# Optimization experiments

Hardware: AMD Instinct MI355X
Metric: run time of the kernel (lower is better)

## Reference

```python
import jax, jax.numpy as jnp
import numpy as np
from jax import lax

THRESHOLD = 0.9


def _conv(x, w, b, stride):
    # x: [B,C,H,W], w: [O,I,3,3] (OIHW)
    y = lax.conv_general_dilated(x, w, (stride, stride), 'SAME',
                                 dimension_numbers=('NCHW', 'OIHW', 'NCHW'))
    return y + b[None, :, None, None]


def _expert(x, w1, b1, w2, b2, wf, bf):
    h = jax.nn.relu(_conv(x, w1, b1, 2))   # [B,64,112,112]
    h = jax.nn.relu(_conv(h, w2, b2, 2))   # [B,128,56,56]
    g = h.mean(axis=(2, 3))                # [B,128] global average pool
    return g @ wf + bf                     # [B,2] logits


def setup_inputs() -> dict:
    key = jax.random.key(0)
    ks = jax.random.split(key, 13)
    f32 = jnp.float32
    def rn(k, shape, scale):
        return jax.random.normal(k, shape, dtype=f32) * scale
    return {
        'x':    rn(ks[0], (64, 3, 224, 224), 1.0),
        't_w1': rn(ks[1], (64, 3, 3, 3),   0.2),
        't_b1': jnp.zeros((64,), f32),
        't_w2': rn(ks[2], (128, 64, 3, 3), 0.05),
        't_b2': jnp.zeros((128,), f32),
        't_wf': rn(ks[3], (128, 2),        0.1),
        't_bf': jnp.zeros((2,), f32),
        'f_w1': rn(ks[4], (64, 3, 3, 3),   0.2),
        'f_b1': jnp.zeros((64,), f32),
        'f_w2': rn(ks[5], (128, 64, 3, 3), 0.05),
        'f_b2': jnp.zeros((128,), f32),
        'f_wf': rn(ks[6], (128, 2),        0.1),
        'f_bf': jnp.zeros((2,), f32),
    }


def reference(x, t_w1, t_b1, t_w2, t_b2, t_wf, t_bf,
              f_w1, f_b1, f_w2, f_b2, f_wf, f_bf):
    t_logits = _expert(x, t_w1, t_b1, t_w2, t_b2, t_wf, t_bf)   # [B,2]
    t_conf = jax.nn.softmax(t_logits, axis=1).max(axis=1)        # [B]
    use_texture2 = t_conf <= THRESHOLD                           # [B] bool
    # jit-friendly dense evaluation of the second expert; the where-mask
    # reproduces the original gather/scatter blend exactly (values and grads).
    f_logits = _expert(x, f_w1, f_b1, f_w2, f_b2, f_wf, f_bf)   # [B,2]
    output = jnp.where(use_texture2[:, None],
                       0.7 * t_logits + 0.3 * f_logits,
                       t_logits)
    freq_usage = use_texture2.astype(jnp.float32).mean()
    return (output, freq_usage)
```

## Files before the change

kernel.cpp:

```cpp
#include <hip/hip_runtime.h>
#include <hip/hip_bf16.h>
#include <math.h>


#define W2B_OFF   0ull
#define W1F_OFF   589824ull
#define G_OFF     606208ull
#define H1_OFF    671744ull
#define H1E_US    52301824ull
#define H1B_US    817216ull
#define WS_NEED   (H1_OFF + 2ull*H1E_US*2ull + 4096ull)

typedef __attribute__((ext_vector_type(8))) short bf16x8;
typedef __attribute__((ext_vector_type(4))) float f32x4;

__device__ inline ushort f2bf(float v) {
  __hip_bfloat16 h = __float2bfloat16(v);
  return *(ushort*)&h;
}
__device__ inline float bf2f(ushort u) {
  __hip_bfloat16 h = *(__hip_bfloat16*)&u;
  return __bfloat162float(h);
}

__global__ __launch_bounds__(256) void prep_new(
    const float* __restrict__ w2_t, const float* __restrict__ w2_f,
    const float* __restrict__ w1_t, const float* __restrict__ w1_f,
    char* __restrict__ ws) {
  int idx = blockIdx.x * 256 + threadIdx.x;
  ushort* w2frag = (ushort*)(ws + W2B_OFF);
  ushort* w1frag = (ushort*)(ws + W1F_OFF);
  if (idx < 294912) {
    int j    = idx & 7;
    int lane = (idx >> 3) & 63;
    int t2   = idx >> 9;
    int kc   = t2 % 18;
    int t3   = t2 / 18;
    int octile = t3 & 7;
    int t4   = t3 >> 3;
    int e    = t4 & 1;
    int term = t4 >> 1;
    int oc = octile * 16 + (lane & 15);
    int kk = kc * 32 + (lane >> 4) * 8 + j;
    int kh = kk / 192, r2 = kk - kh * 192, kw = r2 >> 6, ic = r2 & 63;
    const float* src = e ? w2_f : w2_t;
    float w = src[((oc * 64 + ic) * 3 + kh) * 3 + kw];
    ushort hi = f2bf(w);
    w2frag[idx] = term ? f2bf(w - bf2f(hi)) : hi;
  } else if (idx < 294912 + 8192) {
    int i2   = idx - 294912;
    int j    = i2 & 7;
    int lane = (i2 >> 3) & 63;
    int m    = (i2 >> 9) & 3;
    int term = (i2 >> 11) & 1;
    int e    = (i2 >> 12) & 1;
    int oc = m * 16 + (lane & 15);
    int kk = (lane >> 4) * 8 + j;
    const float* src = e ? w1_f : w1_t;
    float w = (kk < 27) ? src[oc * 27 + kk] : 0.f;
    ushort hi = f2bf(w);
    w1frag[i2] = term ? f2bf(w - bf2f(hi)) : hi;
  }
}

__global__ __launch_bounds__(256) void conv1_mfma(
    const float* __restrict__ x,
    const ushort* __restrict__ w1f_all,
    const float* __restrict__ b1_t, const float* __restrict__ b1_f,
    ushort* __restrict__ h1_all)
{
  const int gR  = blockIdx.x;
  const int b   = blockIdx.y;
  const int e   = blockIdx.z;
  const int tid = threadIdx.x;
  const int w    = tid >> 6;
  const int lane = tid & 63;
  const int q    = lane >> 4;
  const int n    = lane & 15;

  ushort* h1b = h1_all + (size_t)e * H1E_US + (size_t)b * H1B_US;
  const float* b1 = e ? b1_f : b1_t;

  constexpr int CW = 233;
  __shared__ unsigned int xs[3 * 9 * CW];

  const float* xb = x + (size_t)b * 150528;
  const int xr0 = 8 * gR;
  for (int i = tid; i < 1512; i += 256) {
    int ic  = i / 504;
    int rem = i - ic * 504;
    int r   = rem / 56;
    int u   = rem - r * 56;
    int xr  = xr0 + r;
    float4 p = make_float4(0.f, 0.f, 0.f, 0.f);
    if (xr < 224) p = *(const float4*)(xb + (ic * 224 + xr) * 224 + 4 * u);
    float vv[4] = {p.x, p.y, p.z, p.w};
    int base = (ic * 9 + r) * CW + 4 * u;
#pragma unroll
    for (int jj = 0; jj < 4; ++jj) {
      ushort hi = f2bf(vv[jj]);
      ushort lo = f2bf(vv[jj] - bf2f(hi));
      xs[base + jj] = (unsigned int)hi | ((unsigned int)lo << 16);
    }
  }
  if (tid < 27) xs[tid * CW + 224] = 0;

  h1b[((size_t)((4 * gR + (tid >> 6)) * 113 + 112)) * 64 + (tid & 63)] = 0;
  if (gR == 0) {
    unsigned int* z = (unsigned int*)&h1b[(size_t)112 * 113 * 64];
    for (int i = tid; i < 3616; i += 256) z[i] = 0;
  }

  bf16x8 whi[4], wlo[4];
#pragma unroll
  for (int m = 0; m < 4; ++m) {
    whi[m] = *(const bf16x8*)&w1f_all[(((size_t)(e * 2 + 0) * 4 + m) * 64 + lane) * 8];
    wlo[m] = *(const bf16x8*)&w1f_all[(((size_t)(e * 2 + 1) * 4 + m) * 64 + lane) * 8];
  }
  float4 bv[4];
#pragma unroll
  for (int m = 0; m < 4; ++m)
    bv[m] = *(const float4*)&b1[m * 16 + 4 * q];

  int off[8];
#pragma unroll
  for (int j = 0; j < 8; ++j) {
    int kk = q * 8 + j;
    if (kk < 27) {
      int ic = kk / 9;
      int r9 = kk - ic * 9;
      int kh = r9 / 3;
      int kw = r9 - kh * 3;
      off[j] = (ic * 9 + kh) * CW + kw;
    } else {
      off[j] = -1;
    }
  }

  __syncthreads();

  const int row   = 4 * gR + w;
  const int rbase = (2 * w) * CW;

  for (int nt = 0; nt < 7; ++nt) {
    const int c = nt * 16 + n;
    const int base = rbase + 2 * c;
    unsigned int g[8];
#pragma unroll
    for (int j = 0; j < 8; ++j)
      g[j] = (off[j] >= 0) ? xs[base + off[j]] : 0u;
    bf16x8 bhi, blo;
#pragma unroll
    for (int j = 0; j < 8; ++j) {
      bhi[j] = (short)(g[j] & 0xffffu);
      blo[j] = (short)(g[j] >> 16);
    }
    f32x4 acc[4];
#pragma unroll
    for (int m = 0; m < 4; ++m) acc[m] = (f32x4){0.f, 0.f, 0.f, 0.f};
#pragma unroll
    for (int m = 0; m < 4; ++m) {
      acc[m] = __builtin_amdgcn_mfma_f32_16x16x32_bf16(whi[m], bhi, acc[m], 0, 0, 0);
      acc[m] = __builtin_amdgcn_mfma_f32_16x16x32_bf16(wlo[m], bhi, acc[m], 0, 0, 0);
      acc[m] = __builtin_amdgcn_mfma_f32_16x16x32_bf16(whi[m], blo, acc[m], 0, 0, 0);
    }
    size_t po = ((size_t)(row * 113 + c)) * 64 + 4 * q;
#pragma unroll
    for (int m = 0; m < 4; ++m) {
      float v0 = fmaxf(acc[m][0] + bv[m].x, 0.f);
      float v1 = fmaxf(acc[m][1] + bv[m].y, 0.f);
      float v2 = fmaxf(acc[m][2] + bv[m].z, 0.f);
      float v3 = fmaxf(acc[m][3] + bv[m].w, 0.f);
      uint2 uu;
      uu.x = (unsigned int)f2bf(v0) | ((unsigned int)f2bf(v1) << 16);
      uu.y = (unsigned int)f2bf(v2) | ((unsigned int)f2bf(v3) << 16);
      *(uint2*)&h1b[po + m * 16] = uu;
    }
  }
}

__global__ __launch_bounds__(256) void conv2_mfma(
    const ushort* __restrict__ h1_all,
    const ushort* __restrict__ w2frag,
    const float* __restrict__ b2_t, const float* __restrict__ b2_f,
    float* __restrict__ g)
{
  const int T = blockIdx.x;
  const int b = blockIdx.y;
  const int e = blockIdx.z;
  const int tid  = threadIdx.x;
  const int w    = tid >> 6;
  const int lane = tid & 63;
  const ushort* h1b = h1_all + (size_t)e * H1E_US + (size_t)b * H1B_US;
  const float* b2 = e ? b2_f : b2_t;

  __shared__ ushort hs[2 * 113 * 72];

  const int q   = lane >> 4;
  const int n   = lane & 15;
  const int pxl = lane & 7;
  const int rl  = (lane >> 3) & 1;

  f32x4 acc[2][7];
#pragma unroll
  for (int mt = 0; mt < 2; ++mt)
#pragma unroll
    for (int nt = 0; nt < 7; ++nt) acc[mt][nt] = (f32x4){0.f, 0.f, 0.f, 0.f};

  for (int kh = 0; kh < 3; ++kh) {
    __syncthreads();
    for (int i = tid; i < 1808; i += 256) {
      int rs = (i >= 904) ? 1 : 0;
      int rem = i - rs * 904;
      int hx = rem >> 3, gq = rem & 7;
      int R = 4 * T + kh + 2 * rs;
      *(bf16x8*)&hs[(rs * 113 + hx) * 72 + 8 * gq] =
          *(const bf16x8*)&h1b[((size_t)(R * 113 + hx)) * 64 + 8 * gq];
    }
    __syncthreads();
#pragma unroll
    for (int kw = 0; kw < 3; ++kw) {
#pragma unroll
      for (int icc = 0; icc < 2; ++icc) {
        const int kc = kh * 6 + kw * 2 + icc;
        const int icoff = icc * 32 + 8 * q;
        bf16x8 bf[7];
#pragma unroll
        for (int nt = 0; nt < 7; ++nt) {
          int hx = 2 * (8 * nt + pxl) + kw;
          bf[nt] = *(const bf16x8*)&hs[(rl * 113 + hx) * 72 + icoff];
        }
#pragma unroll
        for (int term = 0; term < 2; ++term) {
#pragma unroll
          for (int mt = 0; mt < 2; ++mt) {
            const int octile = 2 * w + mt;
            bf16x8 af = *(const bf16x8*)
                &w2frag[((size_t)(((term * 2 + e) * 8 + octile) * 18 + kc)) * 512
                        + lane * 8];
#pragma unroll
            for (int nt = 0; nt < 7; ++nt)
              acc[mt][nt] = __builtin_amdgcn_mfma_f32_16x16x32_bf16(
                  af, bf[nt], acc[mt][nt], 0, 0, 0);
          }
        }
      }
    }
  }

#pragma unroll
  for (int mt = 0; mt < 2; ++mt) {
#pragma unroll
    for (int reg = 0; reg < 4; ++reg) {
      const int oc = 32 * w + 16 * mt + 4 * q + reg;
      const float bias = b2[oc];
      float s = 0.f;
#pragma unroll
      for (int nt = 0; nt < 7; ++nt) s += fmaxf(acc[mt][nt][reg] + bias, 0.f);
      s += __shfl_xor(s, 1);
      s += __shfl_xor(s, 2);
      s += __shfl_xor(s, 4);
      s += __shfl_xor(s, 8);
      if (n == 0) atomicAdd(&g[((size_t)e * 64 + b) * 128 + oc], s);
    }
  }
}

__global__ __launch_bounds__(64) void finale(
    const float* __restrict__ g,
    const float* __restrict__ t_wf, const float* __restrict__ t_bf,
    const float* __restrict__ f_wf, const float* __restrict__ f_bf,
    float* __restrict__ out)
{
  const int b = threadIdx.x;
  const float inv = 1.0f / 3136.0f;
  const float* gt = g + b * 128;
  const float* gf = g + (64 + b) * 128;
  float lt0 = t_bf[0], lt1 = t_bf[1];
  float lf0 = f_bf[0], lf1 = f_bf[1];
  for (int k = 0; k < 128; ++k) {
    float vt = gt[k] * inv;
    float vf = gf[k] * inv;
    lt0 = fmaf(vt, t_wf[2 * k],     lt0);
    lt1 = fmaf(vt, t_wf[2 * k + 1], lt1);
    lf0 = fmaf(vf, f_wf[2 * k],     lf0);
    lf1 = fmaf(vf, f_wf[2 * k + 1], lf1);
  }
  float m  = fmaxf(lt0, lt1);
  float e0 = expf(lt0 - m), e1 = expf(lt1 - m);
  float conf = fmaxf(e0, e1) / (e0 + e1);
  bool use2 = (conf <= 0.9f);
  out[2 * b]     = use2 ? 0.7f * lt0 + 0.3f * lf0 : lt0;
  out[2 * b + 1] = use2 ? 0.7f * lt1 + 0.3f * lf1 : lt1;
  unsigned long long mask = __ballot(use2);
  if (b == 0) out[128] = (float)__popcll(mask) * (1.0f / 64.0f);
}

__global__ __launch_bounds__(256) void transpose_w2(
    const float* __restrict__ w2_t, const float* __restrict__ w2_f,
    float* __restrict__ w2t) {
  int idx = blockIdx.x * 256 + threadIdx.x;
  int e = idx / 73728;
  int r = idx - e * 73728;
  int k = r >> 7, oc = r & 127;
  const float* src = e ? w2_f : w2_t;
  w2t[idx] = src[oc * 576 + k];
}

__global__ __launch_bounds__(256, 3) void fused_expert(
    const float* __restrict__ x,
    const float* __restrict__ w1_t, const float* __restrict__ b1_t,
    const float* __restrict__ b2_t,
    const float* __restrict__ w1_f, const float* __restrict__ b1_f,
    const float* __restrict__ b2_f,
    const float* __restrict__ w2t_all, float* __restrict__ g)
{
  const int tile = blockIdx.x, b = blockIdx.y, e = blockIdx.z;
  const int ty = tile >> 1, tx = tile & 1;
  const float* w1  = e ? w1_f : w1_t;
  const float* b1  = e ? b1_f : b1_t;
  const float* b2  = e ? b2_f : b2_t;
  const float* w2t = w2t_all + e * 73728;
  __shared__ float x_s[3 * 19 * 116];
  __shared__ float h1_s[8 * 9 * 58];
  __shared__ float w1_s[1728];
  const int tid = threadIdx.x;
  {
    const float* xb = x + (size_t)b * 150528;
    const int xr0 = ty * 16, xc0 = tx * 112;
    for (int idx = tid; idx < 3 * 19 * 116; idx += 256) {
      int ic = idx / (19 * 116);
      int rem = idx - ic * (19 * 116);
      int r = rem / 116, cc = rem - r * 116;
      int xr = xr0 + r, xc = xc0 + cc;
      float v = 0.f;
      if (xr < 224 && xc < 224 && cc < 115) v = xb[(ic * 224 + xr) * 224 + xc];
      x_s[idx] = v;
    }
    for (int idx = tid; idx < 1728; idx += 256) w1_s[idx] = w1[idx];
  }
  const int ocg = tid >> 4, posg = tid & 15;
  int pbase[7];
#pragma unroll
  for (int j = 0; j < 7; ++j) {
    int p = posg + 16 * j, py = p / 28, px = p - py * 28;
    pbase[j] = py * 2 * 58 + px * 2;
  }
  float acc[7][8];
#pragma unroll
  for (int j = 0; j < 7; ++j)
#pragma unroll
    for (int i = 0; i < 8; ++i) acc[j][i] = 0.f;
  const int hc_l = tid >> 5, l32 = tid & 31;
  for (int c = 0; c < 8; ++c) {
    __syncthreads();
    {
      const int hc = c * 8 + hc_l;
      const float bias = b1[hc];
      float wr[27];
#pragma unroll
      for (int qq = 0; qq < 27; ++qq) wr[qq] = w1_s[hc * 27 + qq];
      for (int p = l32; p < 513; p += 32) {
        int hy = p / 57, hx = p - hy * 57;
        float a = bias;
#pragma unroll
        for (int ic = 0; ic < 3; ++ic)
#pragma unroll
          for (int kh = 0; kh < 3; ++kh) {
            const float* row = &x_s[ic * (19 * 116) + (2 * hy + kh) * 116 + 2 * hx];
            a = fmaf(row[0], wr[ic * 9 + kh * 3 + 0], a);
            a = fmaf(row[1], wr[ic * 9 + kh * 3 + 1], a);
            a = fmaf(row[2], wr[ic * 9 + kh * 3 + 2], a);
          }
        float v = fmaxf(a, 0.f);
        int hy_g = ty * 8 + hy, hx_g = tx * 56 + hx;
        if (hy_g >= 112 || hx_g >= 112) v = 0.f;
        h1_s[hc_l * 522 + hy * 58 + hx] = v;
      }
    }
    __syncthreads();
    for (int ic_l = 0; ic_l < 8; ++ic_l) {
#pragma unroll
      for (int kh = 0; kh < 3; ++kh)
#pragma unroll
        for (int kw = 0; kw < 3; ++kw) {
          const int k = (c * 8 + ic_l) * 9 + kh * 3 + kw;
          const float4 wA = *(const float4*)(w2t + k * 128 + ocg * 8);
          const float4 wB = *(const float4*)(w2t + k * 128 + ocg * 8 + 4);
          const float* hp = &h1_s[ic_l * 522 + kh * 58 + kw];
#pragma unroll
          for (int j = 0; j < 7; ++j) {
            float h = hp[pbase[j]];
            acc[j][0] = fmaf(wA.x, h, acc[j][0]);
            acc[j][1] = fmaf(wA.y, h, acc[j][1]);
            acc[j][2] = fmaf(wA.z, h, acc[j][2]);
            acc[j][3] = fmaf(wA.w, h, acc[j][3]);
            acc[j][4] = fmaf(wB.x, h, acc[j][4]);
            acc[j][5] = fmaf(wB.y, h, acc[j][5]);
            acc[j][6] = fmaf(wB.z, h, acc[j][6]);
            acc[j][7] = fmaf(wB.w, h, acc[j][7]);
          }
        }
    }
  }
  __syncthreads();
  float* red = x_s;
#pragma unroll
  for (int i = 0; i < 8; ++i) {
    float bb = b2[ocg * 8 + i];
    float t = 0.f;
#pragma unroll
    for (int j = 0; j < 7; ++j) t += fmaxf(acc[j][i] + bb, 0.f);
    red[posg * 129 + ocg * 8 + i] = t;
  }
  __syncthreads();
  if (tid < 128) {
    float t = 0.f;
#pragma unroll
    for (int pg = 0; pg < 16; ++pg) t += red[pg * 129 + tid];
    atomicAdd(&g[(e * 64 + b) * 128 + tid], t);
  }
}

extern "C" void kernel_launch(void* const* d_in, const int* in_sizes, int n_in,
                              void* d_out, int out_size, void* d_ws, size_t ws_size,
                              hipStream_t stream) {
  const float* x    = (const float*)d_in[0];
  const float* t_w1 = (const float*)d_in[1];
  const float* t_b1 = (const float*)d_in[2];
  const float* t_w2 = (const float*)d_in[3];
  const float* t_b2 = (const float*)d_in[4];
  const float* t_wf = (const float*)d_in[5];
  const float* t_bf = (const float*)d_in[6];
  const float* f_w1 = (const float*)d_in[7];
  const float* f_b1 = (const float*)d_in[8];
  const float* f_w2 = (const float*)d_in[9];
  const float* f_b2 = (const float*)d_in[10];
  const float* f_wf = (const float*)d_in[11];
  const float* f_bf = (const float*)d_in[12];
  float* out = (float*)d_out;
  char* ws = (char*)d_ws;

  if (ws_size >= WS_NEED) {
    float*  gbuf   = (float*)(ws + G_OFF);
    ushort* h1     = (ushort*)(ws + H1_OFF);
    ushort* w2frag = (ushort*)(ws + W2B_OFF);
    ushort* w1f    = (ushort*)(ws + W1F_OFF);
    hipMemsetAsync(gbuf, 0, 2 * 64 * 128 * sizeof(float), stream);
    prep_new<<<1184, 256, 0, stream>>>(t_w2, f_w2, t_w1, f_w1, ws);
    conv1_mfma<<<dim3(28, 64, 2), 256, 0, stream>>>(x, w1f, t_b1, f_b1, h1);
    conv2_mfma<<<dim3(28, 64, 2), 256, 0, stream>>>(h1, w2frag, t_b2, f_b2, gbuf);
    finale<<<1, 64, 0, stream>>>(gbuf, t_wf, t_bf, f_wf, f_bf, out);
  } else {
    float* w2t = (float*)ws;
    float* g2  = (float*)(ws + 589824);
    hipMemsetAsync(g2, 0, 2 * 64 * 128 * sizeof(float), stream);
    transpose_w2<<<576, 256, 0, stream>>>(t_w2, f_w2, w2t);
    fused_expert<<<dim3(28, 64, 2), 256, 0, stream>>>(
        x, t_w1, t_b1, t_b2, f_w1, f_b1, f_b2, w2t, g2);
    finale<<<1, 64, 0, stream>>>(g2, t_wf, t_bf, f_wf, f_bf, out);
  }
}
```

Baseline: 299.3 us.

## Switch split-bf16 MFMA convolutions to single fp16 MFMA and swizzle conv2 LDS

Drops the hi/lo bf16 splitting of weights and activations and uses a single fp16 MFMA pass. That cuts conv1's MFMA count from three passes to one and conv2's from two to one. It also halves the weight prep work and workspace. In conv2 it XOR-swizzles the LDS layout of h1 tiles to reduce bank conflicts on the B-fragment reads. The cost is lower accuracy: a single fp16 pass has fewer mantissa bits than the compensated bf16 scheme, and fp16 has a narrower range that could overflow for larger activations.

```diff
diff --git a/kernel.cpp b/kernel.cpp
--- a/kernel.cpp
+++ b/kernel.cpp
@@ -1,26 +1,23 @@
 #include <hip/hip_runtime.h>
-#include <hip/hip_bf16.h>
+#include <hip/hip_fp16.h>
 #include <math.h>
 
 
 #define W2B_OFF   0ull
-#define W1F_OFF   589824ull
-#define G_OFF     606208ull
-#define H1_OFF    671744ull
+#define W1F_OFF   294912ull
+#define G_OFF     303104ull
+#define H1_OFF    368640ull
 #define H1E_US    52301824ull
 #define H1B_US    817216ull
 #define WS_NEED   (H1_OFF + 2ull*H1E_US*2ull + 4096ull)
 
 typedef __attribute__((ext_vector_type(8))) short bf16x8;
+typedef __attribute__((ext_vector_type(8))) _Float16 half8;
 typedef __attribute__((ext_vector_type(4))) float f32x4;
 
-__device__ inline ushort f2bf(float v) {
-  __hip_bfloat16 h = __float2bfloat16(v);
+__device__ inline ushort f2h(float v) {
+  __half h = __float2half(v);
   return *(ushort*)&h;
-}
-__device__ inline float bf2f(ushort u) {
-  __hip_bfloat16 h = *(__hip_bfloat16*)&u;
-  return __bfloat162float(h);
 }
 
 __global__ __launch_bounds__(256) void prep_new(
@@ -30,36 +27,29 @@
   int idx = blockIdx.x * 256 + threadIdx.x;
   ushort* w2frag = (ushort*)(ws + W2B_OFF);
   ushort* w1frag = (ushort*)(ws + W1F_OFF);
-  if (idx < 294912) {
+  if (idx < 147456) {
     int j    = idx & 7;
     int lane = (idx >> 3) & 63;
     int t2   = idx >> 9;
     int kc   = t2 % 18;
     int t3   = t2 / 18;
     int octile = t3 & 7;
-    int t4   = t3 >> 3;
-    int e    = t4 & 1;
-    int term = t4 >> 1;
+    int e    = t3 >> 3;
     int oc = octile * 16 + (lane & 15);
     int kk = kc * 32 + (lane >> 4) * 8 + j;
     int kh = kk / 192, r2 = kk - kh * 192, kw = r2 >> 6, ic = r2 & 63;
     const float* src = e ? w2_f : w2_t;
-    float w = src[((oc * 64 + ic) * 3 + kh) * 3 + kw];
-    ushort hi = f2bf(w);
-    w2frag[idx] = term ? f2bf(w - bf2f(hi)) : hi;
-  } else if (idx < 294912 + 8192) {
-    int i2   = idx - 294912;
+    w2frag[idx] = f2h(src[((oc * 64 + ic) * 3 + kh) * 3 + kw]);
+  } else if (idx < 147456 + 4096) {
+    int i2   = idx - 147456;
     int j    = i2 & 7;
     int lane = (i2 >> 3) & 63;
     int m    = (i2 >> 9) & 3;
-    int term = (i2 >> 11) & 1;
-    int e    = (i2 >> 12) & 1;
+    int e    = (i2 >> 11) & 1;
     int oc = m * 16 + (lane & 15);
     int kk = (lane >> 4) * 8 + j;
     const float* src = e ? w1_f : w1_t;
-    float w = (kk < 27) ? src[oc * 27 + kk] : 0.f;
-    ushort hi = f2bf(w);
-    w1frag[i2] = term ? f2bf(w - bf2f(hi)) : hi;
+    w1frag[i2] = f2h((kk < 27) ? src[oc * 27 + kk] : 0.f);
   }
 }
 
@@ -94,14 +84,11 @@
     int xr  = xr0 + r;
     float4 p = make_float4(0.f, 0.f, 0.f, 0.f);
     if (xr < 224) p = *(const float4*)(xb + (ic * 224 + xr) * 224 + 4 * u);
-    float vv[4] = {p.x, p.y, p.z, p.w};
     int base = (ic * 9 + r) * CW + 4 * u;
-#pragma unroll
-    for (int jj = 0; jj < 4; ++jj) {
-      ushort hi = f2bf(vv[jj]);
-      ushort lo = f2bf(vv[jj] - bf2f(hi));
-      xs[base + jj] = (unsigned int)hi | ((unsigned int)lo << 16);
-    }
+    xs[base + 0] = (unsigned int)f2h(p.x);
+    xs[base + 1] = (unsigned int)f2h(p.y);
+    xs[base + 2] = (unsigned int)f2h(p.z);
+    xs[base + 3] = (unsigned int)f2h(p.w);
   }
   if (tid < 27) xs[tid * CW + 224] = 0;
 
@@ -111,12 +98,10 @@
     for (int i = tid; i < 3616; i += 256) z[i] = 0;
   }
 
-  bf16x8 whi[4], wlo[4];
-#pragma unroll
-  for (int m = 0; m < 4; ++m) {
-    whi[m] = *(const bf16x8*)&w1f_all[(((size_t)(e * 2 + 0) * 4 + m) * 64 + lane) * 8];
-    wlo[m] = *(const bf16x8*)&w1f_all[(((size_t)(e * 2 + 1) * 4 + m) * 64 + lane) * 8];
-  }
+  half8 wf[4];
+#pragma unroll
+  for (int m = 0; m < 4; ++m)
+    wf[m] = *(const half8*)&w1f_all[(((size_t)(e * 4 + m)) * 64 + lane) * 8];
   float4 bv[4];
 #pragma unroll
   for (int m = 0; m < 4; ++m)
@@ -149,31 +134,26 @@
 #pragma unroll
     for (int j = 0; j < 8; ++j)
       g[j] = (off[j] >= 0) ? xs[base + off[j]] : 0u;
-    bf16x8 bhi, blo;
-#pragma unroll
-    for (int j = 0; j < 8; ++j) {
-      bhi[j] = (short)(g[j] & 0xffffu);
-      blo[j] = (short)(g[j] >> 16);
-    }
+    union { half8 h; unsigned int u[4]; } bh;
+#pragma unroll
+    for (int p = 0; p < 4; ++p)
+      bh.u[p] = (g[2 * p] & 0xffffu) | (g[2 * p + 1] << 16);
     f32x4 acc[4];
 #pragma unroll
     for (int m = 0; m < 4; ++m) acc[m] = (f32x4){0.f, 0.f, 0.f, 0.f};
 #pragma unroll
+    for (int m = 0; m < 4; ++m)
+      acc[m] = __builtin_amdgcn_mfma_f32_16x16x32_f16(wf[m], bh.h, acc[m], 0, 0, 0);
+    size_t po = ((size_t)(row * 113 + c)) * 64 + 4 * q;
+#pragma unroll
     for (int m = 0; m < 4; ++m) {
-      acc[m] = __builtin_amdgcn_mfma_f32_16x16x32_bf16(whi[m], bhi, acc[m], 0, 0, 0);
-      acc[m] = __builtin_amdgcn_mfma_f32_16x16x32_bf16(wlo[m], bhi, acc[m], 0, 0, 0);
-      acc[m] = __builtin_amdgcn_mfma_f32_16x16x32_bf16(whi[m], blo, acc[m], 0, 0, 0);
-    }
-    size_t po = ((size_t)(row * 113 + c)) * 64 + 4 * q;
-#pragma unroll
-    for (int m = 0; m < 4; ++m) {
-      float v0 = fmaxf(acc[m][0] + bv[m].x, 0.f);
-      float v1 = fmaxf(acc[m][1] + bv[m].y, 0.f);
-      float v2 = fmaxf(acc[m][2] + bv[m].z, 0.f);
-      float v3 = fmaxf(acc[m][3] + bv[m].w, 0.f);
+      ushort v0 = f2h(fmaxf(acc[m][0] + bv[m].x, 0.f));
+      ushort v1 = f2h(fmaxf(acc[m][1] + bv[m].y, 0.f));
+      ushort v2 = f2h(fmaxf(acc[m][2] + bv[m].z, 0.f));
+      ushort v3 = f2h(fmaxf(acc[m][3] + bv[m].w, 0.f));
       uint2 uu;
-      uu.x = (unsigned int)f2bf(v0) | ((unsigned int)f2bf(v1) << 16);
-      uu.y = (unsigned int)f2bf(v2) | ((unsigned int)f2bf(v3) << 16);
+      uu.x = (unsigned int)v0 | ((unsigned int)v1 << 16);
+      uu.y = (unsigned int)v2 | ((unsigned int)v3 << 16);
       *(uint2*)&h1b[po + m * 16] = uu;
     }
   }
@@ -214,7 +194,8 @@
       int rem = i - rs * 904;
       int hx = rem >> 3, gq = rem & 7;
       int R = 4 * T + kh + 2 * rs;
-      *(bf16x8*)&hs[(rs * 113 + hx) * 72 + 8 * gq] =
+      int gsw = gq ^ ((hx >> 1) & 7);
+      *(bf16x8*)&hs[(rs * 113 + hx) * 72 + 8 * gsw] =
           *(const bf16x8*)&h1b[((size_t)(R * 113 + hx)) * 64 + 8 * gq];
     }
     __syncthreads();
@@ -223,26 +204,22 @@
 #pragma unroll
       for (int icc = 0; icc < 2; ++icc) {
         const int kc = kh * 6 + kw * 2 + icc;
-        const int icoff = icc * 32 + 8 * q;
-        bf16x8 bf[7];
+        half8 bf[7];
 #pragma unroll
         for (int nt = 0; nt < 7; ++nt) {
           int hx = 2 * (8 * nt + pxl) + kw;
-          bf[nt] = *(const bf16x8*)&hs[(rl * 113 + hx) * 72 + icoff];
+          int gr = (icc * 4 + q) ^ ((hx >> 1) & 7);
+          bf[nt] = *(const half8*)&hs[(rl * 113 + hx) * 72 + 8 * gr];
         }
 #pragma unroll
-        for (int term = 0; term < 2; ++term) {
-#pragma unroll
-          for (int mt = 0; mt < 2; ++mt) {
-            const int octile = 2 * w + mt;
-            bf16x8 af = *(const bf16x8*)
-                &w2frag[((size_t)(((term * 2 + e) * 8 + octile) * 18 + kc)) * 512
-                        + lane * 8];
-#pragma unroll
-            for (int nt = 0; nt < 7; ++nt)
-              acc[mt][nt] = __builtin_amdgcn_mfma_f32_16x16x32_bf16(
-                  af, bf[nt], acc[mt][nt], 0, 0, 0);
-          }
+        for (int mt = 0; mt < 2; ++mt) {
+          const int octile = 2 * w + mt;
+          half8 af = *(const half8*)
+              &w2frag[((size_t)((e * 8 + octile) * 18 + kc)) * 512 + lane * 8];
+#pragma unroll
+          for (int nt = 0; nt < 7; ++nt)
+            acc[mt][nt] = __builtin_amdgcn_mfma_f32_16x16x32_f16(
+                af, bf[nt], acc[mt][nt], 0, 0, 0);
         }
       }
     }
@@ -447,7 +424,7 @@
     ushort* w2frag = (ushort*)(ws + W2B_OFF);
     ushort* w1f    = (ushort*)(ws + W1F_OFF);
     hipMemsetAsync(gbuf, 0, 2 * 64 * 128 * sizeof(float), stream);
-    prep_new<<<1184, 256, 0, stream>>>(t_w2, f_w2, t_w1, f_w1, ws);
+    prep_new<<<592, 256, 0, stream>>>(t_w2, f_w2, t_w1, f_w1, ws);
     conv1_mfma<<<dim3(28, 64, 2), 256, 0, stream>>>(x, w1f, t_b1, f_b1, h1);
     conv2_mfma<<<dim3(28, 64, 2), 256, 0, stream>>>(h1, w2frag, t_b2, f_b2, gbuf);
     finale<<<1, 64, 0, stream>>>(gbuf, t_wf, t_bf, f_wf, f_bf, out);
```

New measurement: 296.9 us. About the same (-0.8%).
